# Kernel optimization log

Measured on AMD Instinct MI355X. Metric: run time of the kernel, lower is better.

The kernel has to match this reference:

```python
import jax, jax.numpy as jnp
import numpy as np

N_NODES = 100000
N_EDGES = 1600000
HID = 64


def _gcn_conv(x, src, dst, W, b, n_nodes):
    """PyG GCNConv: add self-loops, symmetric deg normalization, linear transform.
    out_i = sum_{j in N(i) u {i}} deg_i^{-1/2} deg_j^{-1/2} (x_j W) + b
    """
    h = x @ W  # [N, out] small matmul
    loops = jnp.arange(n_nodes, dtype=src.dtype)
    s = jnp.concatenate([src, loops])  # sources (message senders)
    d = jnp.concatenate([dst, loops])  # targets (aggregation index)
    deg = jax.ops.segment_sum(jnp.ones_like(d, dtype=h.dtype), d, num_segments=n_nodes)
    dinv = jnp.where(deg > 0, jax.lax.rsqrt(deg), 0.0)
    coef = dinv[s] * dinv[d]  # [E+N]
    msg = h[s] * coef[:, None]  # gather + scale (memory-bound)
    out = jax.ops.segment_sum(msg, d, num_segments=n_nodes)  # scatter-add
    return out + b


def setup_inputs() -> dict:
    key = jax.random.key(0)
    ks = jax.random.split(key, 16)
    x = jax.random.normal(ks[0], (N_NODES, 4), dtype=jnp.float32)
    edge_index = jax.random.randint(ks[1], (2, N_EDGES), 0, N_NODES, dtype=jnp.int64)
    s = 0.1
    params = {
        'W1': jax.random.normal(ks[2], (4, HID), dtype=jnp.float32) * s,
        'b1': jnp.zeros((HID,), dtype=jnp.float32),
        'W2': jax.random.normal(ks[3], (HID, HID), dtype=jnp.float32) * s,
        'b2': jnp.zeros((HID,), dtype=jnp.float32),
        'W3': jax.random.normal(ks[4], (HID, HID), dtype=jnp.float32) * s,
        'b3': jnp.zeros((HID,), dtype=jnp.float32),
        'Wp': jax.random.normal(ks[5], (HID, HID), dtype=jnp.float32) * s,
        'bp': jnp.zeros((HID,), dtype=jnp.float32),
        'Wa': jax.random.normal(ks[6], (HID, 4), dtype=jnp.float32) * s,
        'ba': jnp.zeros((4,), dtype=jnp.float32),
        'Wm': jax.random.normal(ks[7], (HID, 2), dtype=jnp.float32) * s,
        'bm': jnp.zeros((2,), dtype=jnp.float32),
        'Wg': jax.random.normal(ks[8], (HID, 3), dtype=jnp.float32) * s,
        'bg': jnp.zeros((3,), dtype=jnp.float32),
        'Wt': jax.random.normal(ks[9], (HID, 10), dtype=jnp.float32) * s,
        'bt': jnp.zeros((10,), dtype=jnp.float32),
    }
    return {'x': x, 'edge_index': edge_index, 'node_index': 0, **params}


def reference(x, edge_index, node_index, W1, b1, W2, b2, W3, b3, Wp, bp, Wa, ba, Wm, bm, Wg, bg, Wt, bt):
    src, dst = edge_index[0], edge_index[1]
    n = x.shape[0]
    # dropout is identity in eval mode
    h = jax.nn.relu(_gcn_conv(x, src, dst, W1, b1, n))
    h = jax.nn.relu(_gcn_conv(h, src, dst, W2, b2, n))
    h = jax.nn.relu(_gcn_conv(h, src, dst, W3, b3, n))
    node = h[node_index]
    node = jax.nn.relu(node @ Wp + bp)
    return (node @ Wa + ba, node @ Wm + bm, node @ Wg + bg, node @ Wt + bt)
```

## Files before the change

### kernel.cpp

```cpp
#include <hip/hip_runtime.h>


#define HID  64
#define CAP1 2048
#define CAP2 512
#define RB1  128
#define RB2  128
#define CL3  2048
#define VE   8

__device__ __forceinline__ int ld_src(const void* ei, int is64, long long e) {
  return is64 ? (int)((const unsigned*)ei)[e << 1] : ((const int*)ei)[e];
}

__device__ __forceinline__ int load_dsts(const void* ei, long long E, long long base,
                                         int is64, int d[VE]) {
  int n = (int)((E - base) < VE ? (E - base) : VE);
  if (is64) {
    const unsigned long long* p = (const unsigned long long*)ei + E + base;
    if (n == VE && (((E + base) & 1) == 0)) {
      const ulonglong2* q = (const ulonglong2*)p;
#pragma unroll
      for (int k = 0; k < VE / 2; ++k) {
        ulonglong2 v = q[k];
        d[2 * k] = (int)(unsigned)v.x; d[2 * k + 1] = (int)(unsigned)v.y;
      }
    } else {
      for (int k = 0; k < n; ++k) d[k] = (int)(unsigned)p[k];
    }
  } else {
    const int* p = (const int*)ei + E + base;
    if (n == VE && (((E + base) & 3) == 0)) {
      const int4* q = (const int4*)p;
#pragma unroll
      for (int k = 0; k < VE / 4; ++k) {
        int4 v = q[k];
        d[4 * k] = v.x; d[4 * k + 1] = v.y; d[4 * k + 2] = v.z; d[4 * k + 3] = v.w;
      }
    } else {
      for (int k = 0; k < n; ++k) d[k] = p[k];
    }
  }
  return n;
}

__global__ void k_detect(const unsigned* e32, int* flag) {
  if (blockIdx.x == 0 && threadIdx.x == 0) {
    int is64 = 1;
    for (int k = 0; k < 64; ++k)
      if (e32[2 * k + 1] != 0u) { is64 = 0; break; }
    *flag = is64;
  }
}

__global__ void k_scanF1(const void* ei, int E, const int* flag, const int* nidx_p,
                         int* slot2, int* node2, int* cnt2, int* l3, int* ec3) {
  long long base = ((long long)blockIdx.x * blockDim.x + threadIdx.x) * VE;
  if (base >= E) return;
  int is64 = *flag, nidx = *nidx_p;
  int d[VE];
  int n = load_dsts(ei, E, base, is64, d);
  for (int k = 0; k < n; ++k) {
    if (d[k] == nidx) {
      int s = ld_src(ei, is64, base + k);
      if (atomicCAS(&slot2[s], -1, -2) == -1) {
        int p = atomicAdd(cnt2, 1) & (CAP2 - 1);
        slot2[s] = p; node2[p] = s;
      }
      int q = atomicAdd(ec3, 1);
      if (q < CL3) l3[q] = s;
    }
  }
}

__global__ void k_seed(const int* nidx_p, int* slot1, int* slot2,
                       int* node1, int* node2, int* need, int* cnt1, int* cnt2) {
  __shared__ int rows;
  if (threadIdx.x == 0) {
    int n = *nidx_p;
    if (atomicCAS(&slot2[n], -1, -2) == -1) {
      int p = atomicAdd(cnt2, 1) & (CAP2 - 1);
      slot2[n] = p; node2[p] = n;
    }
    rows = min(*cnt2, CAP2);
  }
  __syncthreads();
  for (int r = threadIdx.x; r < rows; r += blockDim.x) {
    int i = node2[r];
    need[i] = 1;
    if (atomicCAS(&slot1[i], -1, -2) == -1) {
      int p = atomicAdd(cnt1, 1) & (CAP1 - 1);
      slot1[i] = p; node1[p] = i;
    }
  }
}

__global__ void k_scanF2(const void* ei, int E, const int* flag,
                         const int* slot2, int* slot1, int* node1, int* need,
                         int* cnt1, int* rc2, int* bl2) {
  long long base = ((long long)blockIdx.x * blockDim.x + threadIdx.x) * VE;
  if (base >= E) return;
  int is64 = *flag;
  int d[VE];
  int n = load_dsts(ei, E, base, is64, d);
  for (int k = 0; k < n; ++k) {
    int ad = slot2[d[k]];
    if (ad >= 0) {
      int s = ld_src(ei, is64, base + k);
      need[s] = 1;
      if (atomicCAS(&slot1[s], -1, -2) == -1) {
        int p = atomicAdd(cnt1, 1) & (CAP1 - 1);
        slot1[s] = p; node1[p] = s;
      }
      int q = atomicAdd(&rc2[ad], 1);
      if (q < RB2) bl2[ad * RB2 + q] = s;
    }
  }
}

__global__ void k_scanS(const void* ei, int E, const int* flag,
                        const int* slot1, int* need, int* rc1, int* bl1) {
  long long base = ((long long)blockIdx.x * blockDim.x + threadIdx.x) * VE;
  if (base >= E) return;
  int is64 = *flag;
  int d[VE];
  int n = load_dsts(ei, E, base, is64, d);
  for (int k = 0; k < n; ++k) {
    int ad = slot1[d[k]];
    if (ad >= 0) {
      int s = ld_src(ei, is64, base + k);
      need[s] = 1;
      int q = atomicAdd(&rc1[ad], 1);
      if (q < RB1) bl1[ad * RB1 + q] = s;
    }
  }
}

__global__ void k_scanDeg(const void* ei, int E, const int* flag,
                          const int* need, int* deg) {
  long long base = ((long long)blockIdx.x * blockDim.x + threadIdx.x) * VE;
  if (base >= E) return;
  int is64 = *flag;
  int d[VE];
  int n = load_dsts(ei, E, base, is64, d);
  for (int k = 0; k < n; ++k)
    if (need[d[k]]) atomicAdd(&deg[d[k]], 1);
}

__global__ void k_l1(const float* __restrict__ x, const float* __restrict__ W1,
                     const float* __restrict__ b1, const int* __restrict__ deg,
                     const int* __restrict__ node1, const int* __restrict__ cnt1,
                     const int* __restrict__ rc1, const int* __restrict__ bl1,
                     float* __restrict__ h1c) {
  int w = blockIdx.x * 4 + (threadIdx.x >> 6);
  int lane = threadIdx.x & 63;
  int rows = min(*cnt1, CAP1);
  if (w >= rows) return;
  int i = node1[w];
  float di = 1.0f / sqrtf((float)(deg[i] + 1));
  int cnt = min(rc1[w], RB1);
  float ax = 0.f, ay = 0.f, az = 0.f, aw = 0.f;
  for (int j = lane; j < cnt; j += 64) {
    int s = bl1[w * RB1 + j];
    float c = (1.0f / sqrtf((float)(deg[s] + 1))) * di;
    float4 xv = ((const float4*)x)[s];
    ax += c * xv.x; ay += c * xv.y; az += c * xv.z; aw += c * xv.w;
  }
#pragma unroll
  for (int t = 1; t < 64; t <<= 1) {
    ax += __shfl_xor(ax, t); ay += __shfl_xor(ay, t);
    az += __shfl_xor(az, t); aw += __shfl_xor(aw, t);
  }
  float4 xi = ((const float4*)x)[i];
  float dd = di * di;
  ax += dd * xi.x; ay += dd * xi.y; az += dd * xi.z; aw += dd * xi.w;
  float v = ax * W1[lane] + ay * W1[64 + lane] + az * W1[128 + lane] +
            aw * W1[192 + lane] + b1[lane];
  h1c[w * HID + lane] = v > 0.f ? v : 0.f;
}

__global__ void k_l2(const float* __restrict__ W2, const float* __restrict__ b2,
                     const int* __restrict__ deg, const int* __restrict__ node2,
                     const int* __restrict__ cnt2, const int* __restrict__ slot1,
                     const int* __restrict__ rc2, const int* __restrict__ bl2,
                     const float* __restrict__ h1c, float* __restrict__ h2c) {
  __shared__ float sh[4][HID];
  int wv = threadIdx.x >> 6, lane = threadIdx.x & 63;
  int w = blockIdx.x * 4 + wv;
  int rows = min(*cnt2, CAP2);
  if (w >= rows) return;
  int i = node2[w];
  float di = 1.0f / sqrtf((float)(deg[i] + 1));
  int cnt = min(rc2[w], RB2);
  float acc = 0.f;
  for (int j0 = 0; j0 < cnt; j0 += 64) {
    int nb = min(64, cnt - j0);
    int sl = 0; float c = 0.f;
    if (lane < nb) {
      int s = bl2[w * RB2 + j0 + lane];
      sl = slot1[s];
      c = (1.0f / sqrtf((float)(deg[s] + 1))) * di;
    }
    for (int j = 0; j < nb; ++j) {
      int slj = __shfl(sl, j);
      float cj = __shfl(c, j);
      acc += cj * h1c[slj * HID + lane];
    }
  }
  acc += di * di * h1c[slot1[i] * HID + lane];
  sh[wv][lane] = acc;
  float v = b2[lane];
#pragma unroll 16
  for (int k = 0; k < HID; ++k) v += sh[wv][k] * W2[k * HID + lane];
  h2c[w * HID + lane] = v > 0.f ? v : 0.f;
}

__global__ void k_tail(const int* nidx_p, const int* slot2, const int* deg,
                       const float* h2c, const int* l3, const int* ec3,
                       const float* W3, const float* b3,
                       const float* Wp, const float* bp,
                       const float* Wa, const float* ba,
                       const float* Wm, const float* bm,
                       const float* Wg, const float* bg,
                       const float* Wt, const float* bt, float* out) {
  __shared__ float part[4][HID];
  __shared__ float g3[HID];
  __shared__ float h3[HID];
  __shared__ float p[HID];
  __shared__ int   ssl[64];
  __shared__ float scc[64];
  int tid = threadIdx.x, wv = tid >> 6, lane = tid & 63;
  int nidx = *nidx_p;
  float dn = 1.0f / sqrtf((float)(deg[nidx] + 1));
  int cnt = min(*ec3, CL3);
  float acc = 0.f;
  for (int j0 = 0; j0 < cnt; j0 += 64) {
    int nb = min(64, cnt - j0);
    if (tid < nb) {
      int s = l3[j0 + tid];
      ssl[tid] = slot2[s];
      scc[tid] = (1.0f / sqrtf((float)(deg[s] + 1))) * dn;
    }
    __syncthreads();
    for (int j = wv; j < nb; j += 4)
      acc += scc[j] * h2c[ssl[j] * HID + lane];
    __syncthreads();
  }
  part[wv][lane] = acc;
  __syncthreads();
  if (wv == 0) {
    float a = part[0][lane] + part[1][lane] + part[2][lane] + part[3][lane];
    a += dn * dn * h2c[slot2[nidx] * HID + lane];
    g3[lane] = a;
  }
  __syncthreads();
  if (wv == 0) {
    float v = b3[lane];
#pragma unroll 16
    for (int k = 0; k < HID; ++k) v += g3[k] * W3[k * HID + lane];
    h3[lane] = v > 0.f ? v : 0.f;
  }
  __syncthreads();
  if (wv == 0) {
    float pv = bp[lane];
#pragma unroll 16
    for (int k = 0; k < HID; ++k) pv += h3[k] * Wp[k * HID + lane];
    p[lane] = pv > 0.f ? pv : 0.f;
  }
  __syncthreads();
  if (tid < 4) {
    float o = ba[tid];
    for (int k = 0; k < HID; ++k) o += p[k] * Wa[k * 4 + tid];
    out[tid] = o;
  } else if (tid < 6) {
    int c = tid - 4; float o = bm[c];
    for (int k = 0; k < HID; ++k) o += p[k] * Wm[k * 2 + c];
    out[tid] = o;
  } else if (tid < 9) {
    int c = tid - 6; float o = bg[c];
    for (int k = 0; k < HID; ++k) o += p[k] * Wg[k * 3 + c];
    out[tid] = o;
  } else if (tid < 19) {
    int c = tid - 9; float o = bt[c];
    for (int k = 0; k < HID; ++k) o += p[k] * Wt[k * 10 + c];
    out[tid] = o;
  }
}

extern "C" void kernel_launch(void* const* d_in, const int* in_sizes, int n_in,
                              void* d_out, int out_size, void* d_ws, size_t ws_size,
                              hipStream_t stream) {
  const float* x  = (const float*)d_in[0];
  const void*  ei = d_in[1];
  const int* nidx = (const int*)d_in[2];
  const float* W1 = (const float*)d_in[3];
  const float* b1 = (const float*)d_in[4];
  const float* W2 = (const float*)d_in[5];
  const float* b2 = (const float*)d_in[6];
  const float* W3 = (const float*)d_in[7];
  const float* b3 = (const float*)d_in[8];
  const float* Wp = (const float*)d_in[9];
  const float* bp = (const float*)d_in[10];
  const float* Wa = (const float*)d_in[11];
  const float* ba = (const float*)d_in[12];
  const float* Wm = (const float*)d_in[13];
  const float* bm = (const float*)d_in[14];
  const float* Wg = (const float*)d_in[15];
  const float* bg = (const float*)d_in[16];
  const float* Wt = (const float*)d_in[17];
  const float* bt = (const float*)d_in[18];
  float* out = (float*)d_out;

  int N = in_sizes[0] / 4;
  int E = in_sizes[1] / 2;

  char* w = (char*)d_ws;
  size_t o = 0;
  auto take = [&](size_t bytes) -> void* {
    void* p = w + o;
    o += (bytes + 255) & ~(size_t)255;
    return p;
  };
  size_t zeroBytes = (size_t)(3 + 2 * N + CAP1 + CAP2) * 4;
  int* zr = (int*)take(zeroBytes);
  int* cnt1 = zr + 0;
  int* cnt2 = zr + 1;
  int* ec3  = zr + 2;
  int* deg  = zr + 3;
  int* need = deg + N;
  int* rc1  = need + N;
  int* rc2  = rc1 + CAP1;
  int* slots = (int*)take((size_t)2 * N * 4);
  int* slot1 = slots;
  int* slot2 = slots + N;
  int*   flag  = (int*)take(4);
  int*   node1 = (int*)take((size_t)CAP1 * 4);
  int*   node2 = (int*)take((size_t)CAP2 * 4);
  int*   bl1   = (int*)take((size_t)CAP1 * RB1 * 4);
  int*   bl2   = (int*)take((size_t)CAP2 * RB2 * 4);
  int*   l3    = (int*)take((size_t)CL3 * 4);
  float* h1c   = (float*)take((size_t)CAP1 * HID * 4);
  float* h2c   = (float*)take((size_t)CAP2 * HID * 4);

  int gS = (int)(((long long)E + 256 * VE - 1) / (256 * VE));

  hipMemsetAsync(zr, 0x00, zeroBytes, stream);
  hipMemsetAsync(slots, 0xFF, (size_t)2 * N * 4, stream);
  k_detect <<<1, 64, 0, stream>>>((const unsigned*)ei, flag);
  k_scanF1 <<<gS, 256, 0, stream>>>(ei, E, flag, nidx, slot2, node2, cnt2, l3, ec3);
  k_seed   <<<1, 256, 0, stream>>>(nidx, slot1, slot2, node1, node2, need, cnt1, cnt2);
  k_scanF2 <<<gS, 256, 0, stream>>>(ei, E, flag, slot2, slot1, node1, need, cnt1, rc2, bl2);
  k_scanS  <<<gS, 256, 0, stream>>>(ei, E, flag, slot1, need, rc1, bl1);
  k_scanDeg<<<gS, 256, 0, stream>>>(ei, E, flag, need, deg);
  k_l1     <<<CAP1 / 4, 256, 0, stream>>>(x, W1, b1, deg, node1, cnt1, rc1, bl1, h1c);
  k_l2     <<<CAP2 / 4, 256, 0, stream>>>(W2, b2, deg, node2, cnt2, slot1, rc2, bl2, h1c, h2c);
  k_tail   <<<1, 256, 0, stream>>>(nidx, slot2, deg, h2c, l3, ec3, W3, b3, Wp, bp,
                                   Wa, ba, Wm, bm, Wg, bg, Wt, bt, out);
}
```

Before: 165.4 us.

## Compact destination indices to int32 and fuse detect, seed, layer-2 and tail kernels

The first edge scan now writes a compacted int32 copy of the destination row, so later scans read 4-byte instead of possibly 8-byte indices. The int64 detection becomes a per-wave ballot inside each kernel, and seeding is folded into the first scan and the second scan. Layer 2 and the tail become one single-block kernel that keeps the first 64 layer-2 rows in shared memory. This cuts three launches and some index bandwidth, at the cost of an extra 4·E-byte workspace write and redundant seeding work in every block.

```diff
diff --git a/kernel.cpp b/kernel.cpp
--- a/kernel.cpp
+++ b/kernel.cpp
@@ -8,6 +8,14 @@
 #define RB2  128
 #define CL3  2048
 #define VE   8
+#define TPB  256
+
+__device__ __forceinline__ int detect64(const void* ei) {
+  const unsigned* e32 = (const unsigned*)ei;
+  int lane = threadIdx.x & 63;
+  bool z = (e32[2 * lane + 1] == 0u);
+  return (__ballot(z) == ~0ull) ? 1 : 0;
+}
 
 __device__ __forceinline__ int ld_src(const void* ei, int is64, long long e) {
   return is64 ? (int)((const unsigned*)ei)[e << 1] : ((const int*)ei)[e];
@@ -44,22 +52,40 @@
   return n;
 }
 
-__global__ void k_detect(const unsigned* e32, int* flag) {
+__device__ __forceinline__ int load_dsts32(const int* dst32, long long E,
+                                           long long base, int d[VE]) {
+  int n = (int)((E - base) < VE ? (E - base) : VE);
+  if (n == VE) {
+    int4 a = ((const int4*)(dst32 + base))[0];
+    int4 b = ((const int4*)(dst32 + base))[1];
+    d[0] = a.x; d[1] = a.y; d[2] = a.z; d[3] = a.w;
+    d[4] = b.x; d[5] = b.y; d[6] = b.z; d[7] = b.w;
+  } else {
+    for (int k = 0; k < n; ++k) d[k] = dst32[base + k];
+  }
+  return n;
+}
+
+__global__ void k_scanF1(const void* ei, int E, const int* nidx_p, int* dst32,
+                         int* slot2, int* node2, int* cnt2, int* l3, int* ec3) {
+  int is64 = detect64(ei);
+  int nidx = *nidx_p;
   if (blockIdx.x == 0 && threadIdx.x == 0) {
-    int is64 = 1;
-    for (int k = 0; k < 64; ++k)
-      if (e32[2 * k + 1] != 0u) { is64 = 0; break; }
-    *flag = is64;
-  }
-}
-
-__global__ void k_scanF1(const void* ei, int E, const int* flag, const int* nidx_p,
-                         int* slot2, int* node2, int* cnt2, int* l3, int* ec3) {
-  long long base = ((long long)blockIdx.x * blockDim.x + threadIdx.x) * VE;
+    if (atomicCAS(&slot2[nidx], -1, -2) == -1) {
+      int p = atomicAdd(cnt2, 1) & (CAP2 - 1);
+      slot2[nidx] = p; node2[p] = nidx;
+    }
+  }
+  long long base = ((long long)blockIdx.x * TPB + threadIdx.x) * VE;
   if (base >= E) return;
-  int is64 = *flag, nidx = *nidx_p;
   int d[VE];
   int n = load_dsts(ei, E, base, is64, d);
+  if (n == VE) {
+    ((int4*)(dst32 + base))[0] = make_int4(d[0], d[1], d[2], d[3]);
+    ((int4*)(dst32 + base))[1] = make_int4(d[4], d[5], d[6], d[7]);
+  } else {
+    for (int k = 0; k < n; ++k) dst32[base + k] = d[k];
+  }
   for (int k = 0; k < n; ++k) {
     if (d[k] == nidx) {
       int s = ld_src(ei, is64, base + k);
@@ -73,19 +99,12 @@
   }
 }
 
-__global__ void k_seed(const int* nidx_p, int* slot1, int* slot2,
-                       int* node1, int* node2, int* need, int* cnt1, int* cnt2) {
-  __shared__ int rows;
-  if (threadIdx.x == 0) {
-    int n = *nidx_p;
-    if (atomicCAS(&slot2[n], -1, -2) == -1) {
-      int p = atomicAdd(cnt2, 1) & (CAP2 - 1);
-      slot2[n] = p; node2[p] = n;
-    }
-    rows = min(*cnt2, CAP2);
-  }
-  __syncthreads();
-  for (int r = threadIdx.x; r < rows; r += blockDim.x) {
+__global__ void k_scanF2(const void* ei, int E, const int* dst32,
+                         const int* slot2, const int* node2, const int* cnt2,
+                         int* slot1, int* node1, int* need, int* cnt1,
+                         int* rc2, int* bl2) {
+  int rows2 = min(*cnt2, CAP2);
+  for (int r = threadIdx.x; r < rows2; r += TPB) {
     int i = node2[r];
     need[i] = 1;
     if (atomicCAS(&slot1[i], -1, -2) == -1) {
@@ -93,16 +112,11 @@
       slot1[i] = p; node1[p] = i;
     }
   }
-}
-
-__global__ void k_scanF2(const void* ei, int E, const int* flag,
-                         const int* slot2, int* slot1, int* node1, int* need,
-                         int* cnt1, int* rc2, int* bl2) {
-  long long base = ((long long)blockIdx.x * blockDim.x + threadIdx.x) * VE;
+  int is64 = detect64(ei);
+  long long base = ((long long)blockIdx.x * TPB + threadIdx.x) * VE;
   if (base >= E) return;
-  int is64 = *flag;
   int d[VE];
-  int n = load_dsts(ei, E, base, is64, d);
+  int n = load_dsts32(dst32, E, base, d);
   for (int k = 0; k < n; ++k) {
     int ad = slot2[d[k]];
     if (ad >= 0) {
@@ -118,13 +132,13 @@
   }
 }
 
-__global__ void k_scanS(const void* ei, int E, const int* flag,
+__global__ void k_scanS(const void* ei, int E, const int* dst32,
                         const int* slot1, int* need, int* rc1, int* bl1) {
-  long long base = ((long long)blockIdx.x * blockDim.x + threadIdx.x) * VE;
+  int is64 = detect64(ei);
+  long long base = ((long long)blockIdx.x * TPB + threadIdx.x) * VE;
   if (base >= E) return;
-  int is64 = *flag;
   int d[VE];
-  int n = load_dsts(ei, E, base, is64, d);
+  int n = load_dsts32(dst32, E, base, d);
   for (int k = 0; k < n; ++k) {
     int ad = slot1[d[k]];
     if (ad >= 0) {
@@ -136,13 +150,11 @@
   }
 }
 
-__global__ void k_scanDeg(const void* ei, int E, const int* flag,
-                          const int* need, int* deg) {
-  long long base = ((long long)blockIdx.x * blockDim.x + threadIdx.x) * VE;
+__global__ void k_scanDeg(int E, const int* dst32, const int* need, int* deg) {
+  long long base = ((long long)blockIdx.x * TPB + threadIdx.x) * VE;
   if (base >= E) return;
-  int is64 = *flag;
   int d[VE];
-  int n = load_dsts(ei, E, base, is64, d);
+  int n = load_dsts32(dst32, E, base, d);
   for (int k = 0; k < n; ++k)
     if (need[d[k]]) atomicAdd(&deg[d[k]], 1);
 }
@@ -179,58 +191,52 @@
   h1c[w * HID + lane] = v > 0.f ? v : 0.f;
 }
 
-__global__ void k_l2(const float* __restrict__ W2, const float* __restrict__ b2,
-                     const int* __restrict__ deg, const int* __restrict__ node2,
-                     const int* __restrict__ cnt2, const int* __restrict__ slot1,
-                     const int* __restrict__ rc2, const int* __restrict__ bl2,
-                     const float* __restrict__ h1c, float* __restrict__ h2c) {
-  __shared__ float sh[4][HID];
-  int wv = threadIdx.x >> 6, lane = threadIdx.x & 63;
-  int w = blockIdx.x * 4 + wv;
-  int rows = min(*cnt2, CAP2);
-  if (w >= rows) return;
-  int i = node2[w];
-  float di = 1.0f / sqrtf((float)(deg[i] + 1));
-  int cnt = min(rc2[w], RB2);
-  float acc = 0.f;
-  for (int j0 = 0; j0 < cnt; j0 += 64) {
-    int nb = min(64, cnt - j0);
-    int sl = 0; float c = 0.f;
-    if (lane < nb) {
-      int s = bl2[w * RB2 + j0 + lane];
-      sl = slot1[s];
-      c = (1.0f / sqrtf((float)(deg[s] + 1))) * di;
-    }
-    for (int j = 0; j < nb; ++j) {
-      int slj = __shfl(sl, j);
-      float cj = __shfl(c, j);
-      acc += cj * h1c[slj * HID + lane];
-    }
-  }
-  acc += di * di * h1c[slot1[i] * HID + lane];
-  sh[wv][lane] = acc;
-  float v = b2[lane];
-#pragma unroll 16
-  for (int k = 0; k < HID; ++k) v += sh[wv][k] * W2[k * HID + lane];
-  h2c[w * HID + lane] = v > 0.f ? v : 0.f;
-}
-
-__global__ void k_tail(const int* nidx_p, const int* slot2, const int* deg,
-                       const float* h2c, const int* l3, const int* ec3,
-                       const float* W3, const float* b3,
-                       const float* Wp, const float* bp,
-                       const float* Wa, const float* ba,
-                       const float* Wm, const float* bm,
-                       const float* Wg, const float* bg,
-                       const float* Wt, const float* bt, float* out) {
-  __shared__ float part[4][HID];
+__global__ __launch_bounds__(TPB) void k_l2tail(
+    const float* W2, const float* b2, const int* deg,
+    const int* node2, const int* cnt2, const int* slot1,
+    const int* rc2, const int* bl2, const float* h1c, float* h2c,
+    const int* nidx_p, const int* slot2, const int* l3, const int* ec3,
+    const float* W3, const float* b3, const float* Wp, const float* bp,
+    const float* Wa, const float* ba, const float* Wm, const float* bm,
+    const float* Wg, const float* bg, const float* Wt, const float* bt,
+    float* out) {
+  __shared__ float h2s[64][HID];
+  __shared__ float smA[4][HID];
   __shared__ float g3[HID];
-  __shared__ float h3[HID];
-  __shared__ float p[HID];
+  __shared__ float h3v[HID];
+  __shared__ float pj[HID];
   __shared__ int   ssl[64];
   __shared__ float scc[64];
   int tid = threadIdx.x, wv = tid >> 6, lane = tid & 63;
   int nidx = *nidx_p;
+  int rows = min(*cnt2, CAP2);
+
+  for (int w = wv; w < rows; w += 4) {
+    int i = node2[w];
+    float di = 1.0f / sqrtf((float)(deg[i] + 1));
+    int cnt = min(rc2[w], RB2);
+    float acc = 0.f;
+    for (int j0 = 0; j0 < cnt; j0 += 64) {
+      int nb = min(64, cnt - j0);
+      int sl = 0; float c = 0.f;
+      if (lane < nb) {
+        int s = bl2[w * RB2 + j0 + lane];
+        sl = slot1[s];
+        c = (1.0f / sqrtf((float)(deg[s] + 1))) * di;
+      }
+      for (int j = 0; j < nb; ++j)
+        acc += __shfl(c, j) * h1c[__shfl(sl, j) * HID + lane];
+    }
+    acc += di * di * h1c[slot1[i] * HID + lane];
+    smA[wv][lane] = acc;
+    float v = b2[lane];
+#pragma unroll 16
+    for (int k = 0; k < HID; ++k) v += smA[wv][k] * W2[k * HID + lane];
+    v = v > 0.f ? v : 0.f;
+    if (w < 64) h2s[w][lane] = v; else h2c[w * HID + lane] = v;
+  }
+  __syncthreads();
+
   float dn = 1.0f / sqrtf((float)(deg[nidx] + 1));
   int cnt = min(*ec3, CL3);
   float acc = 0.f;
@@ -242,47 +248,51 @@
       scc[tid] = (1.0f / sqrtf((float)(deg[s] + 1))) * dn;
     }
     __syncthreads();
-    for (int j = wv; j < nb; j += 4)
-      acc += scc[j] * h2c[ssl[j] * HID + lane];
+    for (int j = wv; j < nb; j += 4) {
+      int r = ssl[j];
+      float hv = (r < 64) ? h2s[r][lane] : h2c[r * HID + lane];
+      acc += scc[j] * hv;
+    }
     __syncthreads();
   }
-  part[wv][lane] = acc;
+  smA[wv][lane] = acc;
   __syncthreads();
   if (wv == 0) {
-    float a = part[0][lane] + part[1][lane] + part[2][lane] + part[3][lane];
-    a += dn * dn * h2c[slot2[nidx] * HID + lane];
-    g3[lane] = a;
+    int r = slot2[nidx];
+    float hv = (r < 64) ? h2s[r][lane] : h2c[r * HID + lane];
+    g3[lane] = smA[0][lane] + smA[1][lane] + smA[2][lane] + smA[3][lane] +
+               dn * dn * hv;
   }
   __syncthreads();
   if (wv == 0) {
     float v = b3[lane];
 #pragma unroll 16
     for (int k = 0; k < HID; ++k) v += g3[k] * W3[k * HID + lane];
-    h3[lane] = v > 0.f ? v : 0.f;
+    h3v[lane] = v > 0.f ? v : 0.f;
   }
   __syncthreads();
   if (wv == 0) {
-    float pv = bp[lane];
+    float v = bp[lane];
 #pragma unroll 16
-    for (int k = 0; k < HID; ++k) pv += h3[k] * Wp[k * HID + lane];
-    p[lane] = pv > 0.f ? pv : 0.f;
+    for (int k = 0; k < HID; ++k) v += h3v[k] * Wp[k * HID + lane];
+    pj[lane] = v > 0.f ? v : 0.f;
   }
   __syncthreads();
   if (tid < 4) {
     float o = ba[tid];
-    for (int k = 0; k < HID; ++k) o += p[k] * Wa[k * 4 + tid];
+    for (int k = 0; k < HID; ++k) o += pj[k] * Wa[k * 4 + tid];
     out[tid] = o;
   } else if (tid < 6) {
     int c = tid - 4; float o = bm[c];
-    for (int k = 0; k < HID; ++k) o += p[k] * Wm[k * 2 + c];
+    for (int k = 0; k < HID; ++k) o += pj[k] * Wm[k * 2 + c];
     out[tid] = o;
   } else if (tid < 9) {
     int c = tid - 6; float o = bg[c];
-    for (int k = 0; k < HID; ++k) o += p[k] * Wg[k * 3 + c];
+    for (int k = 0; k < HID; ++k) o += pj[k] * Wg[k * 3 + c];
     out[tid] = o;
   } else if (tid < 19) {
     int c = tid - 9; float o = bt[c];
-    for (int k = 0; k < HID; ++k) o += p[k] * Wt[k * 10 + c];
+    for (int k = 0; k < HID; ++k) o += pj[k] * Wt[k * 10 + c];
     out[tid] = o;
   }
 }
@@ -333,7 +343,7 @@
   int* slots = (int*)take((size_t)2 * N * 4);
   int* slot1 = slots;
   int* slot2 = slots + N;
-  int*   flag  = (int*)take(4);
+  int*   dst32 = (int*)take((size_t)E * 4);
   int*   node1 = (int*)take((size_t)CAP1 * 4);
   int*   node2 = (int*)take((size_t)CAP2 * 4);
   int*   bl1   = (int*)take((size_t)CAP1 * RB1 * 4);
@@ -342,18 +352,17 @@
   float* h1c   = (float*)take((size_t)CAP1 * HID * 4);
   float* h2c   = (float*)take((size_t)CAP2 * HID * 4);
 
-  int gS = (int)(((long long)E + 256 * VE - 1) / (256 * VE));
+  int gS = (int)(((long long)E + TPB * VE - 1) / (TPB * VE));
 
   hipMemsetAsync(zr, 0x00, zeroBytes, stream);
   hipMemsetAsync(slots, 0xFF, (size_t)2 * N * 4, stream);
-  k_detect <<<1, 64, 0, stream>>>((const unsigned*)ei, flag);
-  k_scanF1 <<<gS, 256, 0, stream>>>(ei, E, flag, nidx, slot2, node2, cnt2, l3, ec3);
-  k_seed   <<<1, 256, 0, stream>>>(nidx, slot1, slot2, node1, node2, need, cnt1, cnt2);
-  k_scanF2 <<<gS, 256, 0, stream>>>(ei, E, flag, slot2, slot1, node1, need, cnt1, rc2, bl2);
-  k_scanS  <<<gS, 256, 0, stream>>>(ei, E, flag, slot1, need, rc1, bl1);
-  k_scanDeg<<<gS, 256, 0, stream>>>(ei, E, flag, need, deg);
-  k_l1     <<<CAP1 / 4, 256, 0, stream>>>(x, W1, b1, deg, node1, cnt1, rc1, bl1, h1c);
-  k_l2     <<<CAP2 / 4, 256, 0, stream>>>(W2, b2, deg, node2, cnt2, slot1, rc2, bl2, h1c, h2c);
-  k_tail   <<<1, 256, 0, stream>>>(nidx, slot2, deg, h2c, l3, ec3, W3, b3, Wp, bp,
-                                   Wa, ba, Wm, bm, Wg, bg, Wt, bt, out);
-}
+  k_scanF1 <<<gS, TPB, 0, stream>>>(ei, E, nidx, dst32, slot2, node2, cnt2, l3, ec3);
+  k_scanF2 <<<gS, TPB, 0, stream>>>(ei, E, dst32, slot2, node2, cnt2,
+                                    slot1, node1, need, cnt1, rc2, bl2);
+  k_scanS  <<<gS, TPB, 0, stream>>>(ei, E, dst32, slot1, need, rc1, bl1);
+  k_scanDeg<<<gS, TPB, 0, stream>>>(E, dst32, need, deg);
+  k_l1     <<<CAP1 / 4, TPB, 0, stream>>>(x, W1, b1, deg, node1, cnt1, rc1, bl1, h1c);
+  k_l2tail <<<1, TPB, 0, stream>>>(W2, b2, deg, node2, cnt2, slot1, rc2, bl2,
+                                   h1c, h2c, nidx, slot2, l3, ec3, W3, b3,
+                                   Wp, bp, Wa, ba, Wm, bm, Wg, bg, Wt, bt, out);
+}
```

Result: slower. 194.3 us (+17.5%).
